# Kernel optimization log

Hardware: AMD Instinct MI355X
Metric: run time of the kernel (lower is better)

The kernel has to match this reference:

```python
import jax, jax.numpy as jnp
import numpy as np

D = 1  # dilation


def _unfold3x3(x, d):
    # x: [B, C, H, W] -> [B, H*W, 9, C]; matches torch.nn.Unfold(kernel_size=3,
    # dilation=d, padding=d, stride=1) followed by the module's reshapes.
    B, C, H, W = x.shape
    xp = jnp.pad(x, ((0, 0), (0, 0), (d, d), (d, d)))
    pats = [xp[:, :, i * d:i * d + H, j * d:j * d + W] for i in range(3) for j in range(3)]
    p = jnp.stack(pats, axis=0)  # [9, B, C, H, W], kernel positions row-major (center = 4)
    return p.transpose(1, 3, 4, 0, 2).reshape(B, H * W, 9, C)


def _masked_bn(h, m, gamma, beta, eps=1e-5):
    # BatchNorm1d in training mode applied only to rows selected by bool mask m
    # (the torch code gathers rows, BNs them, scatters back into zeros).
    # Stats are the biased mean/var over the selected rows, per channel.
    axes = tuple(range(h.ndim - 1))
    mf = m[..., None].astype(h.dtype)
    n = jnp.maximum(mf.sum(), 1.0)
    mean = (h * mf).sum(axes) / n
    var = (((h - mean) ** 2 * mf)).sum(axes) / n
    return (h - mean) * jax.lax.rsqrt(var + eps) * gamma + beta


def setup_inputs() -> dict:
    key = jax.random.key(0)
    ks = jax.random.split(key, 8)
    B, H, W = 2, 64, 1024
    Cin, Cout, Cm = 64, 64, 4
    s = 0.1
    x = jax.random.normal(ks[0], (B, Cm + Cin, H, W), jnp.float32)
    mask = (jax.random.uniform(ks[1], (B, 1, H, W)) > 0.3).astype(jnp.float32)
    return {
        "x": x,
        "mask": mask,
        "w1": jax.random.normal(ks[2], (8, Cm), jnp.float32) * s,
        "bn1_g": jnp.ones(8, jnp.float32),
        "bn1_b": jnp.zeros(8, jnp.float32),
        "w2": jax.random.normal(ks[3], (1, 8), jnp.float32) * s,
        "b2": jnp.zeros(1, jnp.float32),
        "g1": jax.random.normal(ks[4], (8, Cm), jnp.float32) * s,
        "gbn1_g": jnp.ones(8, jnp.float32),
        "gbn1_b": jnp.zeros(8, jnp.float32),
        "g2": jax.random.normal(ks[5], (8, 8), jnp.float32) * s,
        "gbn2_g": jnp.ones(8, jnp.float32),
        "gbn2_b": jnp.zeros(8, jnp.float32),
        "w_agg": jax.random.normal(ks[6], (Cout, 72 + Cin), jnp.float32) * s,
        "abn_g": jnp.ones(Cout, jnp.float32),
        "abn_b": jnp.zeros(Cout, jnp.float32),
    }


def reference(x, mask, w1, bn1_g, bn1_b, w2, b2, g1, gbn1_g, gbn1_b, g2, gbn2_g, gbn2_b, w_agg, abn_g, abn_b):
    B, C, H, W = x.shape
    xu = _unfold3x3(x, D)                      # [B, HW, 9, C]
    mu = _unfold3x3(mask, D)[..., 0]           # [B, HW, 9]
    msel = mu > 0                              # valid-neighbor mask
    mp0 = msel[:, :, 4]                        # valid-center mask [B, HW]
    pn = xu[..., :4] - xu[:, :, 4:5, :4]       # relative meta coords [B, HW, 9, 4]
    feats = xu[..., 4:]                        # neighbor features [B, HW, 9, Cin]

    # weight branch (dense compute + mask == torch's gather/scatter)
    h = _masked_bn(pn @ w1.T, msel, bn1_g, bn1_b)
    h = jax.nn.relu(h) @ w2.T + b2             # [B, HW, 9, 1]
    wts = jnp.where(msel, h[..., 0], 0.0)      # zeros at invalid neighbors pre-softmax
    wts = jax.nn.softmax(wts, axis=-1)[..., None]

    fagg = (wts * feats).sum(axis=2)           # [B, HW, Cin]

    # geo branch
    g = jax.nn.relu(_masked_bn(pn @ g1.T, msel, gbn1_g, gbn1_b))
    g = jax.nn.relu(_masked_bn(g @ g2.T, msel, gbn2_g, gbn2_b))
    g = jnp.where(msel[..., None], g, 0.0)
    g = (wts * g).reshape(B, H * W, 72)

    # aggregation over valid centers
    out = jnp.concatenate([fagg, g], axis=-1) @ w_agg.T
    out = jax.nn.relu(_masked_bn(out, mp0, abn_g, abn_b))
    out = jnp.where(mp0[..., None], out, 0.0)  # [B, HW, Cout]
    return out.transpose(0, 2, 1).reshape(B, -1, H, W)  # fold with k=1 == reshape
```

## Files before the change

kernel.cpp:

```cpp
#include <hip/hip_runtime.h>

#define HW_ 65536
#define W_ 1024
#define H_ 64
#define B_ 2
#define C_ 68
#define NPIX 131072
#define EPS 1e-5f

typedef __attribute__((ext_vector_type(8))) short short8;
typedef __attribute__((ext_vector_type(4))) float floatx4;

__device__ __forceinline__ unsigned short f2bf(float f) {
  unsigned u = __float_as_uint(f);
  u += 0x7fffu + ((u >> 16) & 1u);
  return (unsigned short)(u >> 16);
}
__device__ __forceinline__ unsigned pack2(float a, float b) {
  return (unsigned)f2bf(a) | ((unsigned)f2bf(b) << 16);
}
__device__ __forceinline__ float wred(float v) {
  v += __shfl_xor(v, 1);  v += __shfl_xor(v, 2);  v += __shfl_xor(v, 4);
  v += __shfl_xor(v, 8);  v += __shfl_xor(v, 16); v += __shfl_xor(v, 32);
  return v;
}
__device__ __forceinline__ int swz_tile(int bid) {
  return (bid & 7) * 64 + (bid >> 3);
}

__global__ __launch_bounds__(256) void k_stats1(
    const float* __restrict__ x, const float* __restrict__ mask,
    const float* __restrict__ w1, const float* __restrict__ g1,
    float* __restrict__ ws) {
  float acc[34];
#pragma unroll
  for (int i = 0; i < 34; i++) acc[i] = 0.f;

  int p = swz_tile(blockIdx.x) * 256 + threadIdx.x;
  {
    int b = p >> 16, s = p & (HW_ - 1);
    int h = s >> 10, w = s & (W_ - 1);
    const float* xb = x + (size_t)b * C_ * HW_;
    const float* mb = mask + (size_t)b * HW_;
    float xc0 = xb[s], xc1 = xb[HW_ + s], xc2 = xb[2 * HW_ + s], xc3 = xb[3 * HW_ + s];
    acc[33] += (mb[s] > 0.f) ? 1.f : 0.f;
#pragma unroll
    for (int k = 0; k < 9; k++) {
      int di = k / 3 - 1, dj = k % 3 - 1;
      int hh = h + di, ww = w + dj;
      bool inb = ((unsigned)hh < (unsigned)H_) && ((unsigned)ww < (unsigned)W_);
      int ns = hh * W_ + ww;
      float mval = inb ? mb[ns] : 0.f;
      if (mval > 0.f) {
        float pn0 = xb[ns] - xc0;
        float pn1 = xb[HW_ + ns] - xc1;
        float pn2 = xb[2 * HW_ + ns] - xc2;
        float pn3 = xb[3 * HW_ + ns] - xc3;
        acc[32] += 1.f;
#pragma unroll
        for (int o = 0; o < 8; o++) {
          float ta = pn0 * w1[o * 4] + pn1 * w1[o * 4 + 1] + pn2 * w1[o * 4 + 2] + pn3 * w1[o * 4 + 3];
          acc[o] += ta; acc[8 + o] += ta * ta;
          float tg = pn0 * g1[o * 4] + pn1 * g1[o * 4 + 1] + pn2 * g1[o * 4 + 2] + pn3 * g1[o * 4 + 3];
          acc[16 + o] += tg; acc[24 + o] += tg * tg;
        }
      }
    }
  }
  __shared__ float red[4][34];
  int lane = threadIdx.x & 63, wave = threadIdx.x >> 6;
#pragma unroll
  for (int i = 0; i < 34; i++) {
    float r = wred(acc[i]);
    if (lane == 0) red[wave][i] = r;
  }
  __syncthreads();
  if (threadIdx.x < 34)
    atomicAdd(&ws[threadIdx.x],
              red[0][threadIdx.x] + red[1][threadIdx.x] + red[2][threadIdx.x] + red[3][threadIdx.x]);
}

__global__ __launch_bounds__(256) void k_stats2(
    const float* __restrict__ x, const float* __restrict__ mask,
    const float* __restrict__ g1, const float* __restrict__ gbn1_g,
    const float* __restrict__ gbn1_b, const float* __restrict__ g2,
    float* __restrict__ ws) {
  __shared__ float sc[8], sh[8];
  if (threadIdx.x < 8) {
    int o = threadIdx.x;
    float n = fmaxf(ws[32], 1.f);
    float mean = ws[16 + o] / n;
    float var = ws[24 + o] / n - mean * mean;
    float s = gbn1_g[o] * rsqrtf(var + EPS);
    sc[o] = s; sh[o] = gbn1_b[o] - mean * s;
  }
  __syncthreads();

  float acc[16];
#pragma unroll
  for (int i = 0; i < 16; i++) acc[i] = 0.f;

  int p = swz_tile(blockIdx.x) * 256 + threadIdx.x;
  {
    int b = p >> 16, s = p & (HW_ - 1);
    int h = s >> 10, w = s & (W_ - 1);
    const float* xb = x + (size_t)b * C_ * HW_;
    const float* mb = mask + (size_t)b * HW_;
    float xc0 = xb[s], xc1 = xb[HW_ + s], xc2 = xb[2 * HW_ + s], xc3 = xb[3 * HW_ + s];
#pragma unroll
    for (int k = 0; k < 9; k++) {
      int di = k / 3 - 1, dj = k % 3 - 1;
      int hh = h + di, ww = w + dj;
      bool inb = ((unsigned)hh < (unsigned)H_) && ((unsigned)ww < (unsigned)W_);
      int ns = hh * W_ + ww;
      float mval = inb ? mb[ns] : 0.f;
      if (mval > 0.f) {
        float pn0 = xb[ns] - xc0;
        float pn1 = xb[HW_ + ns] - xc1;
        float pn2 = xb[2 * HW_ + ns] - xc2;
        float pn3 = xb[3 * HW_ + ns] - xc3;
        float gb[8];
#pragma unroll
        for (int o = 0; o < 8; o++) {
          float tg = pn0 * g1[o * 4] + pn1 * g1[o * 4 + 1] + pn2 * g1[o * 4 + 2] + pn3 * g1[o * 4 + 3];
          gb[o] = fmaxf(sc[o] * tg + sh[o], 0.f);
        }
#pragma unroll
        for (int j = 0; j < 8; j++) {
          float t2 = 0.f;
#pragma unroll
          for (int o = 0; o < 8; o++) t2 += gb[o] * g2[j * 8 + o];
          acc[j] += t2; acc[8 + j] += t2 * t2;
        }
      }
    }
  }
  __shared__ float red[4][16];
  int lane = threadIdx.x & 63, wave = threadIdx.x >> 6;
#pragma unroll
  for (int i = 0; i < 16; i++) {
    float r = wred(acc[i]);
    if (lane == 0) red[wave][i] = r;
  }
  __syncthreads();
  if (threadIdx.x < 16)
    atomicAdd(&ws[40 + threadIdx.x],
              red[0][threadIdx.x] + red[1][threadIdx.x] + red[2][threadIdx.x] + red[3][threadIdx.x]);
}

__global__ __launch_bounds__(256) void k_fused(
    const float* __restrict__ x, const float* __restrict__ mask,
    const float* __restrict__ w1, const float* __restrict__ bn1_g,
    const float* __restrict__ bn1_b, const float* __restrict__ w2,
    const float* __restrict__ b2, const float* __restrict__ g1,
    const float* __restrict__ gbn1_g, const float* __restrict__ gbn1_b,
    const float* __restrict__ g2, const float* __restrict__ gbn2_g,
    const float* __restrict__ gbn2_b, const float* __restrict__ w_agg,
    const float* __restrict__ ws, float* __restrict__ out_pre,
    float* __restrict__ wsum) {
  __shared__ uint4 vecA[17][256];
  __shared__ float sA[8], hA[8], sG1[8], hG1[8], sG2[8], hG2[8];

  if (threadIdx.x < 24) {
    int o = threadIdx.x & 7;
    float n = fmaxf(ws[32], 1.f);
    float sum, sum2, gma, bta;
    if (threadIdx.x < 8)       { sum = ws[o];      sum2 = ws[8 + o];  gma = bn1_g[o];  bta = bn1_b[o]; }
    else if (threadIdx.x < 16) { sum = ws[16 + o]; sum2 = ws[24 + o]; gma = gbn1_g[o]; bta = gbn1_b[o]; }
    else                       { sum = ws[40 + o]; sum2 = ws[48 + o]; gma = gbn2_g[o]; bta = gbn2_b[o]; }
    float mean = sum / n, var = sum2 / n - mean * mean;
    float s = gma * rsqrtf(var + EPS);
    float sft = bta - mean * s;
    if (threadIdx.x < 8)       { sA[o] = s;  hA[o] = sft; }
    else if (threadIdx.x < 16) { sG1[o] = s; hG1[o] = sft; }
    else                       { sG2[o] = s; hG2[o] = sft; }
  }
  __syncthreads();

  int tile = swz_tile(blockIdx.x);
  int p0 = tile * 256;
  int p = p0 + threadIdx.x;
  int b = p >> 16, s = p & (HW_ - 1);
  int h = s >> 10, w = s & (W_ - 1);
  const float* xb = x + (size_t)b * C_ * HW_;
  const float* mb = mask + (size_t)b * HW_;
  float xc0 = xb[s], xc1 = xb[HW_ + s], xc2 = xb[2 * HW_ + s], xc3 = xb[3 * HW_ + s];
  float b2v = b2[0];

  float ev[9]; int nsv[9]; bool inbv[9], mselv[9];
  float mx = -1e30f;
#pragma unroll
  for (int k = 0; k < 9; k++) {
    int di = k / 3 - 1, dj = k % 3 - 1;
    int hh = h + di, ww = w + dj;
    bool inb = ((unsigned)hh < (unsigned)H_) && ((unsigned)ww < (unsigned)W_);
    int ns = hh * W_ + ww;
    inbv[k] = inb; nsv[k] = ns;
    float mval = inb ? mb[ns] : 0.f;
    bool msel = mval > 0.f;
    mselv[k] = msel;
    float wp = 0.f;
    if (msel) {
      float pn0 = xb[ns] - xc0;
      float pn1 = xb[HW_ + ns] - xc1;
      float pn2 = xb[2 * HW_ + ns] - xc2;
      float pn3 = xb[3 * HW_ + ns] - xc3;
      float accw = 0.f;
#pragma unroll
      for (int o = 0; o < 8; o++) {
        float ta = pn0 * w1[o * 4] + pn1 * w1[o * 4 + 1] + pn2 * w1[o * 4 + 2] + pn3 * w1[o * 4 + 3];
        accw += fmaxf(sA[o] * ta + hA[o], 0.f) * w2[o];
      }
      wp = accw + b2v;
    }
    ev[k] = wp;
    mx = fmaxf(mx, wp);
  }
  float den = 0.f;
#pragma unroll
  for (int k = 0; k < 9; k++) { ev[k] = __expf(ev[k] - mx); den += ev[k]; }
  float inv = 1.f / den;

  float fagg[64];
#pragma unroll
  for (int c = 0; c < 64; c++) fagg[c] = 0.f;

#pragma unroll
  for (int k = 0; k < 9; k++) {
    float wt = ev[k] * inv;
    int ns = nsv[k];
    uint4 pk; pk.x = pk.y = pk.z = pk.w = 0u;
    if (mselv[k]) {
      float pn0 = xb[ns] - xc0;
      float pn1 = xb[HW_ + ns] - xc1;
      float pn2 = xb[2 * HW_ + ns] - xc2;
      float pn3 = xb[3 * HW_ + ns] - xc3;
      float gb[8];
#pragma unroll
      for (int o = 0; o < 8; o++) {
        float tg = pn0 * g1[o * 4] + pn1 * g1[o * 4 + 1] + pn2 * g1[o * 4 + 2] + pn3 * g1[o * 4 + 3];
        gb[o] = fmaxf(sG1[o] * tg + hG1[o], 0.f);
      }
      float gv[8];
#pragma unroll
      for (int j = 0; j < 8; j++) {
        float t2 = 0.f;
#pragma unroll
        for (int o = 0; o < 8; o++) t2 += gb[o] * g2[j * 8 + o];
        float gg = fmaxf(sG2[j] * t2 + hG2[j], 0.f);
        gv[j] = wt * gg;
      }
      pk.x = pack2(gv[0], gv[1]); pk.y = pack2(gv[2], gv[3]);
      pk.z = pack2(gv[4], gv[5]); pk.w = pack2(gv[6], gv[7]);
    }
    vecA[8 + k][threadIdx.x] = pk;
    if (inbv[k]) {
      const float* xf = xb + 4 * HW_ + ns;
#pragma unroll
      for (int c = 0; c < 64; c++) fagg[c] += wt * xf[c * HW_];
    }
  }
#pragma unroll
  for (int c = 0; c < 64; c += 8) {
    uint4 pk;
    pk.x = pack2(fagg[c], fagg[c + 1]);     pk.y = pack2(fagg[c + 2], fagg[c + 3]);
    pk.z = pack2(fagg[c + 4], fagg[c + 5]); pk.w = pack2(fagg[c + 6], fagg[c + 7]);
    vecA[c >> 3][threadIdx.x] = pk;
  }
  __syncthreads();

  int lane = threadIdx.x & 63, wave = threadIdx.x >> 6;
  int q = lane >> 4, r = lane & 15;

  short8 Bf[4][5];
#pragma unroll
  for (int nt = 0; nt < 4; nt++) {
    int n = nt * 16 + r;
#pragma unroll
    for (int ks = 0; ks < 5; ks++) {
      int k0 = ks * 32 + q * 8;
      uint4 pk; pk.x = pk.y = pk.z = pk.w = 0u;
      if (k0 < 136) {
        float4 f0 = *reinterpret_cast<const float4*>(w_agg + n * 136 + k0);
        float4 f1 = *reinterpret_cast<const float4*>(w_agg + n * 136 + k0 + 4);
        pk.x = pack2(f0.x, f0.y); pk.y = pack2(f0.z, f0.w);
        pk.z = pack2(f1.x, f1.y); pk.w = pack2(f1.z, f1.w);
      }
      Bf[nt][ks] = *reinterpret_cast<short8*>(&pk);
    }
  }

  floatx4 acc[4][4];
#pragma unroll
  for (int m = 0; m < 4; m++)
#pragma unroll
    for (int nt = 0; nt < 4; nt++) acc[m][nt] = (floatx4){0.f, 0.f, 0.f, 0.f};

#pragma unroll
  for (int m = 0; m < 4; m++) {
    int mt = wave * 4 + m;
    int pix = mt * 16 + r;
    short8 Af[5];
#pragma unroll
    for (int ks = 0; ks < 5; ks++) {
      int chunk = ks * 4 + q;
      if (chunk < 17)
        Af[ks] = *reinterpret_cast<const short8*>(&vecA[chunk][pix]);
      else
        Af[ks] = (short8){0, 0, 0, 0, 0, 0, 0, 0};
    }
#pragma unroll
    for (int nt = 0; nt < 4; nt++)
#pragma unroll
      for (int ks = 0; ks < 5; ks++)
        acc[m][nt] = __builtin_amdgcn_mfma_f32_16x16x32_bf16(Af[ks], Bf[nt][ks], acc[m][nt], 0, 0, 0);
  }

  float aS[4] = {0.f, 0.f, 0.f, 0.f}, aQ[4] = {0.f, 0.f, 0.f, 0.f};
  int s0 = p0 & (HW_ - 1);
#pragma unroll
  for (int m = 0; m < 4; m++) {
    int mt = wave * 4 + m;
    int srow = s0 + mt * 16 + q * 4;
    float4 mv = *reinterpret_cast<const float4*>(mb + srow);
    float m0 = (mv.x > 0.f) ? 1.f : 0.f, m1 = (mv.y > 0.f) ? 1.f : 0.f;
    float m2 = (mv.z > 0.f) ? 1.f : 0.f, m3 = (mv.w > 0.f) ? 1.f : 0.f;
#pragma unroll
    for (int nt = 0; nt < 4; nt++) {
      int ch = nt * 16 + r;
      float4 ov;
      ov.x = acc[m][nt][0]; ov.y = acc[m][nt][1];
      ov.z = acc[m][nt][2]; ov.w = acc[m][nt][3];
      aS[nt] += ov.x * m0 + ov.y * m1 + ov.z * m2 + ov.w * m3;
      aQ[nt] += ov.x * ov.x * m0 + ov.y * ov.y * m1 + ov.z * ov.z * m2 + ov.w * ov.w * m3;
      *reinterpret_cast<float4*>(out_pre + ((size_t)(b * 64 + ch)) * HW_ + srow) = ov;
    }
  }

  __syncthreads();
  float* rS = (float*)&vecA[0][0];
  float* rQ = rS + 256;
#pragma unroll
  for (int nt = 0; nt < 4; nt++) {
    float v1 = aS[nt], v2 = aQ[nt];
    v1 += __shfl_xor(v1, 16); v1 += __shfl_xor(v1, 32);
    v2 += __shfl_xor(v2, 16); v2 += __shfl_xor(v2, 32);
    if (lane < 16) { rS[wave * 64 + nt * 16 + lane] = v1; rQ[wave * 64 + nt * 16 + lane] = v2; }
  }
  __syncthreads();
  if (threadIdx.x < 64) {
    atomicAdd(&wsum[64 + threadIdx.x],
              rS[threadIdx.x] + rS[64 + threadIdx.x] + rS[128 + threadIdx.x] + rS[192 + threadIdx.x]);
    atomicAdd(&wsum[128 + threadIdx.x],
              rQ[threadIdx.x] + rQ[64 + threadIdx.x] + rQ[128 + threadIdx.x] + rQ[192 + threadIdx.x]);
  }
}

__global__ __launch_bounds__(256) void k_final(
    const float* __restrict__ out_pre, const float* __restrict__ mask,
    const float* __restrict__ abn_g, const float* __restrict__ abn_b,
    const float* __restrict__ ws, float* __restrict__ out) {
  __shared__ float sc[64], sh[64];
  if (threadIdx.x < 64) {
    int c = threadIdx.x;
    float n0 = fmaxf(ws[33], 1.f);
    float mean = ws[64 + c] / n0;
    float var = ws[128 + c] / n0 - mean * mean;
    float s = abn_g[c] * rsqrtf(var + EPS);
    sc[c] = s; sh[c] = abn_b[c] - mean * s;
  }
  __syncthreads();
  int i4 = (blockIdx.x * 256 + threadIdx.x) * 4;
  if (i4 >= B_ * 64 * HW_) return;
  int c = (i4 >> 16) & 63;
  int b = i4 >> 22;
  int s = i4 & (HW_ - 1);
  float4 v = *reinterpret_cast<const float4*>(out_pre + i4);
  float4 m = *reinterpret_cast<const float4*>(mask + (size_t)b * HW_ + s);
  float4 o;
  o.x = (m.x > 0.f) ? fmaxf(v.x * sc[c] + sh[c], 0.f) : 0.f;
  o.y = (m.y > 0.f) ? fmaxf(v.y * sc[c] + sh[c], 0.f) : 0.f;
  o.z = (m.z > 0.f) ? fmaxf(v.z * sc[c] + sh[c], 0.f) : 0.f;
  o.w = (m.w > 0.f) ? fmaxf(v.w * sc[c] + sh[c], 0.f) : 0.f;
  *reinterpret_cast<float4*>(out + i4) = o;
}

extern "C" void kernel_launch(void* const* d_in, const int* in_sizes, int n_in,
                              void* d_out, int out_size, void* d_ws, size_t ws_size,
                              hipStream_t stream) {
  const float* x      = (const float*)d_in[0];
  const float* mask   = (const float*)d_in[1];
  const float* w1     = (const float*)d_in[2];
  const float* bn1_g  = (const float*)d_in[3];
  const float* bn1_b  = (const float*)d_in[4];
  const float* w2     = (const float*)d_in[5];
  const float* b2     = (const float*)d_in[6];
  const float* g1     = (const float*)d_in[7];
  const float* gbn1_g = (const float*)d_in[8];
  const float* gbn1_b = (const float*)d_in[9];
  const float* g2     = (const float*)d_in[10];
  const float* gbn2_g = (const float*)d_in[11];
  const float* gbn2_b = (const float*)d_in[12];
  const float* w_agg  = (const float*)d_in[13];
  const float* abn_g  = (const float*)d_in[14];
  const float* abn_b  = (const float*)d_in[15];
  float* out = (float*)d_out;

  size_t need = 1024 + (size_t)NPIX * 64 * 4;
  if (ws_size < need) return;

  float* wsf = (float*)d_ws;
  float* out_pre = (float*)((char*)d_ws + 1024);

  hipMemsetAsync(d_ws, 0, 1024, stream);
  k_stats1<<<512, 256, 0, stream>>>(x, mask, w1, g1, wsf);
  k_stats2<<<512, 256, 0, stream>>>(x, mask, g1, gbn1_g, gbn1_b, g2, wsf);
  k_fused<<<512, 256, 0, stream>>>(x, mask, w1, bn1_g, bn1_b, w2, b2, g1,
                                   gbn1_g, gbn1_b, g2, gbn2_g, gbn2_b, w_agg,
                                   wsf, out_pre, wsf);
  k_final<<<8192, 256, 0, stream>>>(out_pre, mask, abn_g, abn_b, wsf, out);
}
```

Measured before the change: 222.9 us.

## Store intermediate in bf16, split fused tile across half-blocks, drop atomics for stats

Several changes at once. The pre-BN aggregation output is now stored as bf16 instead of fp32, halving that intermediate's write and read traffic. Stats kernels write per-block partials instead of atomics, and each block handles both batches for the same pixel. The masking branches become branchless multiply-by-mask. The fused kernel now uses 128-pixel tiles with two half-blocks splitting neighbor and channel work and the MFMA N dimension. The bf16 intermediate adds rounding error before batch norm, and the branchless form does extra arithmetic on invalid neighbors.

```diff
diff --git a/kernel.cpp b/kernel.cpp
--- a/kernel.cpp
+++ b/kernel.cpp
@@ -8,6 +8,7 @@
 #define NPIX 131072
 #define EPS 1e-5f
 
+
 typedef __attribute__((ext_vector_type(8))) short short8;
 typedef __attribute__((ext_vector_type(4))) float floatx4;
 
@@ -19,13 +20,13 @@
 __device__ __forceinline__ unsigned pack2(float a, float b) {
   return (unsigned)f2bf(a) | ((unsigned)f2bf(b) << 16);
 }
+__device__ __forceinline__ float bf2f(unsigned short u) {
+  return __uint_as_float(((unsigned)u) << 16);
+}
 __device__ __forceinline__ float wred(float v) {
   v += __shfl_xor(v, 1);  v += __shfl_xor(v, 2);  v += __shfl_xor(v, 4);
   v += __shfl_xor(v, 8);  v += __shfl_xor(v, 16); v += __shfl_xor(v, 32);
   return v;
-}
-__device__ __forceinline__ int swz_tile(int bid) {
-  return (bid & 7) * 64 + (bid >> 3);
 }
 
 __global__ __launch_bounds__(256) void k_stats1(
@@ -36,9 +37,11 @@
 #pragma unroll
   for (int i = 0; i < 34; i++) acc[i] = 0.f;
 
-  int p = swz_tile(blockIdx.x) * 256 + threadIdx.x;
-  {
-    int b = p >> 16, s = p & (HW_ - 1);
+  int t = blockIdx.x * 256 + threadIdx.x;
+#pragma unroll
+  for (int pp = 0; pp < 2; pp++) {
+    int s = t;
+    int b = pp;
     int h = s >> 10, w = s & (W_ - 1);
     const float* xb = x + (size_t)b * C_ * HW_;
     const float* mb = mask + (size_t)b * HW_;
@@ -49,21 +52,20 @@
       int di = k / 3 - 1, dj = k % 3 - 1;
       int hh = h + di, ww = w + dj;
       bool inb = ((unsigned)hh < (unsigned)H_) && ((unsigned)ww < (unsigned)W_);
-      int ns = hh * W_ + ww;
-      float mval = inb ? mb[ns] : 0.f;
-      if (mval > 0.f) {
-        float pn0 = xb[ns] - xc0;
-        float pn1 = xb[HW_ + ns] - xc1;
-        float pn2 = xb[2 * HW_ + ns] - xc2;
-        float pn3 = xb[3 * HW_ + ns] - xc3;
-        acc[32] += 1.f;
-#pragma unroll
-        for (int o = 0; o < 8; o++) {
-          float ta = pn0 * w1[o * 4] + pn1 * w1[o * 4 + 1] + pn2 * w1[o * 4 + 2] + pn3 * w1[o * 4 + 3];
-          acc[o] += ta; acc[8 + o] += ta * ta;
-          float tg = pn0 * g1[o * 4] + pn1 * g1[o * 4 + 1] + pn2 * g1[o * 4 + 2] + pn3 * g1[o * 4 + 3];
-          acc[16 + o] += tg; acc[24 + o] += tg * tg;
-        }
+      int ns = inb ? hh * W_ + ww : s;
+      float mv = mb[ns];
+      float mk = (inb && mv > 0.f) ? 1.f : 0.f;
+      float pn0 = xb[ns] - xc0;
+      float pn1 = xb[HW_ + ns] - xc1;
+      float pn2 = xb[2 * HW_ + ns] - xc2;
+      float pn3 = xb[3 * HW_ + ns] - xc3;
+      acc[32] += mk;
+#pragma unroll
+      for (int o = 0; o < 8; o++) {
+        float ta = pn0 * w1[o * 4] + pn1 * w1[o * 4 + 1] + pn2 * w1[o * 4 + 2] + pn3 * w1[o * 4 + 3];
+        acc[o] += mk * ta; acc[8 + o] += mk * ta * ta;
+        float tg = pn0 * g1[o * 4] + pn1 * g1[o * 4 + 1] + pn2 * g1[o * 4 + 2] + pn3 * g1[o * 4 + 3];
+        acc[16 + o] += mk * tg; acc[24 + o] += mk * tg * tg;
       }
     }
   }
@@ -76,8 +78,8 @@
   }
   __syncthreads();
   if (threadIdx.x < 34)
-    atomicAdd(&ws[threadIdx.x],
-              red[0][threadIdx.x] + red[1][threadIdx.x] + red[2][threadIdx.x] + red[3][threadIdx.x]);
+    ws[threadIdx.x * 256 + blockIdx.x] =
+        red[0][threadIdx.x] + red[1][threadIdx.x] + red[2][threadIdx.x] + red[3][threadIdx.x];
 }
 
 __global__ __launch_bounds__(256) void k_stats2(
@@ -85,12 +87,21 @@
     const float* __restrict__ g1, const float* __restrict__ gbn1_g,
     const float* __restrict__ gbn1_b, const float* __restrict__ g2,
     float* __restrict__ ws) {
+  int lane = threadIdx.x & 63, wave = threadIdx.x >> 6;
+  __shared__ float stat[33];
+  for (int i = 16 + wave; i < 33; i += 4) {
+    const float* src = ws + i * 256;
+    float v = src[lane] + src[64 + lane] + src[128 + lane] + src[192 + lane];
+    v = wred(v);
+    if (lane == 0) stat[i] = v;
+  }
+  __syncthreads();
   __shared__ float sc[8], sh[8];
   if (threadIdx.x < 8) {
     int o = threadIdx.x;
-    float n = fmaxf(ws[32], 1.f);
-    float mean = ws[16 + o] / n;
-    float var = ws[24 + o] / n - mean * mean;
+    float n = fmaxf(stat[32], 1.f);
+    float mean = stat[16 + o] / n;
+    float var = stat[24 + o] / n - mean * mean;
     float s = gbn1_g[o] * rsqrtf(var + EPS);
     sc[o] = s; sh[o] = gbn1_b[o] - mean * s;
   }
@@ -100,9 +111,11 @@
 #pragma unroll
   for (int i = 0; i < 16; i++) acc[i] = 0.f;
 
-  int p = swz_tile(blockIdx.x) * 256 + threadIdx.x;
-  {
-    int b = p >> 16, s = p & (HW_ - 1);
+  int t = blockIdx.x * 256 + threadIdx.x;
+#pragma unroll
+  for (int pp = 0; pp < 2; pp++) {
+    int s = t;
+    int b = pp;
     int h = s >> 10, w = s & (W_ - 1);
     const float* xb = x + (size_t)b * C_ * HW_;
     const float* mb = mask + (size_t)b * HW_;
@@ -112,31 +125,29 @@
       int di = k / 3 - 1, dj = k % 3 - 1;
       int hh = h + di, ww = w + dj;
       bool inb = ((unsigned)hh < (unsigned)H_) && ((unsigned)ww < (unsigned)W_);
-      int ns = hh * W_ + ww;
-      float mval = inb ? mb[ns] : 0.f;
-      if (mval > 0.f) {
-        float pn0 = xb[ns] - xc0;
-        float pn1 = xb[HW_ + ns] - xc1;
-        float pn2 = xb[2 * HW_ + ns] - xc2;
-        float pn3 = xb[3 * HW_ + ns] - xc3;
-        float gb[8];
-#pragma unroll
-        for (int o = 0; o < 8; o++) {
-          float tg = pn0 * g1[o * 4] + pn1 * g1[o * 4 + 1] + pn2 * g1[o * 4 + 2] + pn3 * g1[o * 4 + 3];
-          gb[o] = fmaxf(sc[o] * tg + sh[o], 0.f);
-        }
-#pragma unroll
-        for (int j = 0; j < 8; j++) {
-          float t2 = 0.f;
-#pragma unroll
-          for (int o = 0; o < 8; o++) t2 += gb[o] * g2[j * 8 + o];
-          acc[j] += t2; acc[8 + j] += t2 * t2;
-        }
+      int ns = inb ? hh * W_ + ww : s;
+      float mv = mb[ns];
+      float mk = (inb && mv > 0.f) ? 1.f : 0.f;
+      float pn0 = xb[ns] - xc0;
+      float pn1 = xb[HW_ + ns] - xc1;
+      float pn2 = xb[2 * HW_ + ns] - xc2;
+      float pn3 = xb[3 * HW_ + ns] - xc3;
+      float gb[8];
+#pragma unroll
+      for (int o = 0; o < 8; o++) {
+        float tg = pn0 * g1[o * 4] + pn1 * g1[o * 4 + 1] + pn2 * g1[o * 4 + 2] + pn3 * g1[o * 4 + 3];
+        gb[o] = fmaxf(sc[o] * tg + sh[o], 0.f);
+      }
+#pragma unroll
+      for (int j = 0; j < 8; j++) {
+        float t2 = 0.f;
+#pragma unroll
+        for (int o = 0; o < 8; o++) t2 += gb[o] * g2[j * 8 + o];
+        acc[j] += mk * t2; acc[8 + j] += mk * t2 * t2;
       }
     }
   }
   __shared__ float red[4][16];
-  int lane = threadIdx.x & 63, wave = threadIdx.x >> 6;
 #pragma unroll
   for (int i = 0; i < 16; i++) {
     float r = wred(acc[i]);
@@ -144,8 +155,8 @@
   }
   __syncthreads();
   if (threadIdx.x < 16)
-    atomicAdd(&ws[40 + threadIdx.x],
-              red[0][threadIdx.x] + red[1][threadIdx.x] + red[2][threadIdx.x] + red[3][threadIdx.x]);
+    ws[8704 + threadIdx.x * 256 + blockIdx.x] =
+        red[0][threadIdx.x] + red[1][threadIdx.x] + red[2][threadIdx.x] + red[3][threadIdx.x];
 }
 
 __global__ __launch_bounds__(256) void k_fused(
@@ -153,21 +164,29 @@
     const float* __restrict__ w1, const float* __restrict__ bn1_g,
     const float* __restrict__ bn1_b, const float* __restrict__ w2,
     const float* __restrict__ b2, const float* __restrict__ g1,
-    const float* __restrict__ gbn1_g, const float* __restrict__ gbn1_b,
-    const float* __restrict__ g2, const float* __restrict__ gbn2_g,
+    const float* __restrict__ g2, const float* __restrict__ gbn1_g,
+    const float* __restrict__ gbn1_b, const float* __restrict__ gbn2_g,
     const float* __restrict__ gbn2_b, const float* __restrict__ w_agg,
-    const float* __restrict__ ws, float* __restrict__ out_pre,
-    float* __restrict__ wsum) {
-  __shared__ uint4 vecA[17][256];
+    float* __restrict__ ws, unsigned short* __restrict__ out_pre) {
+  __shared__ uint4 vecT[17][128];
+  __shared__ float stat[50];
   __shared__ float sA[8], hA[8], sG1[8], hG1[8], sG2[8], hG2[8];
 
+  int lane = threadIdx.x & 63, wave = threadIdx.x >> 6;
+  for (int i = wave; i < 50; i += 4) {
+    const float* src = (i < 34) ? (ws + i * 256) : (ws + 8704 + (i - 34) * 256);
+    float v = src[lane] + src[64 + lane] + src[128 + lane] + src[192 + lane];
+    v = wred(v);
+    if (lane == 0) stat[i] = v;
+  }
+  __syncthreads();
   if (threadIdx.x < 24) {
     int o = threadIdx.x & 7;
-    float n = fmaxf(ws[32], 1.f);
+    float n = fmaxf(stat[32], 1.f);
     float sum, sum2, gma, bta;
-    if (threadIdx.x < 8)       { sum = ws[o];      sum2 = ws[8 + o];  gma = bn1_g[o];  bta = bn1_b[o]; }
-    else if (threadIdx.x < 16) { sum = ws[16 + o]; sum2 = ws[24 + o]; gma = gbn1_g[o]; bta = gbn1_b[o]; }
-    else                       { sum = ws[40 + o]; sum2 = ws[48 + o]; gma = gbn2_g[o]; bta = gbn2_b[o]; }
+    if (threadIdx.x < 8)       { sum = stat[o];      sum2 = stat[8 + o];  gma = bn1_g[o];  bta = bn1_b[o]; }
+    else if (threadIdx.x < 16) { sum = stat[16 + o]; sum2 = stat[24 + o]; gma = gbn1_g[o]; bta = gbn1_b[o]; }
+    else                       { sum = stat[34 + o]; sum2 = stat[42 + o]; gma = gbn2_g[o]; bta = gbn2_b[o]; }
     float mean = sum / n, var = sum2 / n - mean * mean;
     float s = gma * rsqrtf(var + EPS);
     float sft = bta - mean * s;
@@ -177,42 +196,42 @@
   }
   __syncthreads();
 
-  int tile = swz_tile(blockIdx.x);
-  int p0 = tile * 256;
-  int p = p0 + threadIdx.x;
-  int b = p >> 16, s = p & (HW_ - 1);
+  int tile = (blockIdx.x & 7) * 128 + (blockIdx.x >> 3);
+  int b = tile >> 9;
+  int s0 = (tile & 511) * 128;
+  int px = threadIdx.x & 127;
+  int half = threadIdx.x >> 7;
+  int s = s0 + px;
   int h = s >> 10, w = s & (W_ - 1);
   const float* xb = x + (size_t)b * C_ * HW_;
   const float* mb = mask + (size_t)b * HW_;
   float xc0 = xb[s], xc1 = xb[HW_ + s], xc2 = xb[2 * HW_ + s], xc3 = xb[3 * HW_ + s];
   float b2v = b2[0];
 
-  float ev[9]; int nsv[9]; bool inbv[9], mselv[9];
+  float ev[9], mkv[9], ibv[9]; int nsv[9];
   float mx = -1e30f;
 #pragma unroll
   for (int k = 0; k < 9; k++) {
     int di = k / 3 - 1, dj = k % 3 - 1;
     int hh = h + di, ww = w + dj;
     bool inb = ((unsigned)hh < (unsigned)H_) && ((unsigned)ww < (unsigned)W_);
-    int ns = hh * W_ + ww;
-    inbv[k] = inb; nsv[k] = ns;
-    float mval = inb ? mb[ns] : 0.f;
-    bool msel = mval > 0.f;
-    mselv[k] = msel;
-    float wp = 0.f;
-    if (msel) {
-      float pn0 = xb[ns] - xc0;
-      float pn1 = xb[HW_ + ns] - xc1;
-      float pn2 = xb[2 * HW_ + ns] - xc2;
-      float pn3 = xb[3 * HW_ + ns] - xc3;
-      float accw = 0.f;
-#pragma unroll
-      for (int o = 0; o < 8; o++) {
-        float ta = pn0 * w1[o * 4] + pn1 * w1[o * 4 + 1] + pn2 * w1[o * 4 + 2] + pn3 * w1[o * 4 + 3];
-        accw += fmaxf(sA[o] * ta + hA[o], 0.f) * w2[o];
-      }
-      wp = accw + b2v;
-    }
+    int ns = inb ? hh * W_ + ww : s;
+    nsv[k] = ns;
+    ibv[k] = inb ? 1.f : 0.f;
+    float mv = mb[ns];
+    float mk = (inb && mv > 0.f) ? 1.f : 0.f;
+    mkv[k] = mk;
+    float pn0 = xb[ns] - xc0;
+    float pn1 = xb[HW_ + ns] - xc1;
+    float pn2 = xb[2 * HW_ + ns] - xc2;
+    float pn3 = xb[3 * HW_ + ns] - xc3;
+    float accw = 0.f;
+#pragma unroll
+    for (int o = 0; o < 8; o++) {
+      float ta = pn0 * w1[o * 4] + pn1 * w1[o * 4 + 1] + pn2 * w1[o * 4 + 2] + pn3 * w1[o * 4 + 3];
+      accw += fmaxf(sA[o] * ta + hA[o], 0.f) * w2[o];
+    }
+    float wp = mk * (accw + b2v);
     ev[k] = wp;
     mx = fmaxf(mx, wp);
   }
@@ -220,17 +239,18 @@
 #pragma unroll
   for (int k = 0; k < 9; k++) { ev[k] = __expf(ev[k] - mx); den += ev[k]; }
   float inv = 1.f / den;
-
-  float fagg[64];
-#pragma unroll
-  for (int c = 0; c < 64; c++) fagg[c] = 0.f;
-
+  float wgv[9], wfv[9];
 #pragma unroll
   for (int k = 0; k < 9; k++) {
     float wt = ev[k] * inv;
-    int ns = nsv[k];
-    uint4 pk; pk.x = pk.y = pk.z = pk.w = 0u;
-    if (mselv[k]) {
+    wgv[k] = wt * mkv[k];
+    wfv[k] = wt * ibv[k];
+  }
+
+#pragma unroll
+  for (int k = 0; k < 9; k++) {
+    if ((k < 4) == (half == 0)) {
+      int ns = nsv[k];
       float pn0 = xb[ns] - xc0;
       float pn1 = xb[HW_ + ns] - xc1;
       float pn2 = xb[2 * HW_ + ns] - xc2;
@@ -241,41 +261,49 @@
         float tg = pn0 * g1[o * 4] + pn1 * g1[o * 4 + 1] + pn2 * g1[o * 4 + 2] + pn3 * g1[o * 4 + 3];
         gb[o] = fmaxf(sG1[o] * tg + hG1[o], 0.f);
       }
+      float wg = wgv[k];
       float gv[8];
 #pragma unroll
       for (int j = 0; j < 8; j++) {
         float t2 = 0.f;
 #pragma unroll
         for (int o = 0; o < 8; o++) t2 += gb[o] * g2[j * 8 + o];
-        float gg = fmaxf(sG2[j] * t2 + hG2[j], 0.f);
-        gv[j] = wt * gg;
-      }
+        gv[j] = wg * fmaxf(sG2[j] * t2 + hG2[j], 0.f);
+      }
+      uint4 pk;
       pk.x = pack2(gv[0], gv[1]); pk.y = pack2(gv[2], gv[3]);
       pk.z = pack2(gv[4], gv[5]); pk.w = pack2(gv[6], gv[7]);
-    }
-    vecA[8 + k][threadIdx.x] = pk;
-    if (inbv[k]) {
-      const float* xf = xb + 4 * HW_ + ns;
-#pragma unroll
-      for (int c = 0; c < 64; c++) fagg[c] += wt * xf[c * HW_];
-    }
-  }
-#pragma unroll
-  for (int c = 0; c < 64; c += 8) {
+      vecT[8 + k][px] = pk;
+    }
+  }
+
+  float fa[32];
+#pragma unroll
+  for (int c = 0; c < 32; c++) fa[c] = 0.f;
+  const float* xf0 = xb + (size_t)(4 + half * 32) * HW_;
+#pragma unroll
+  for (int k = 0; k < 9; k++) {
+    float wf = wfv[k];
+    const float* xf = xf0 + nsv[k];
+#pragma unroll
+    for (int c = 0; c < 32; c++) fa[c] += wf * xf[c * HW_];
+  }
+#pragma unroll
+  for (int c = 0; c < 32; c += 8) {
     uint4 pk;
-    pk.x = pack2(fagg[c], fagg[c + 1]);     pk.y = pack2(fagg[c + 2], fagg[c + 3]);
-    pk.z = pack2(fagg[c + 4], fagg[c + 5]); pk.w = pack2(fagg[c + 6], fagg[c + 7]);
-    vecA[c >> 3][threadIdx.x] = pk;
-  }
-  __syncthreads();
-
-  int lane = threadIdx.x & 63, wave = threadIdx.x >> 6;
+    pk.x = pack2(fa[c], fa[c + 1]);     pk.y = pack2(fa[c + 2], fa[c + 3]);
+    pk.z = pack2(fa[c + 4], fa[c + 5]); pk.w = pack2(fa[c + 6], fa[c + 7]);
+    vecT[half * 4 + (c >> 3)][px] = pk;
+  }
+  __syncthreads();
+
   int q = lane >> 4, r = lane & 15;
-
-  short8 Bf[4][5];
-#pragma unroll
-  for (int nt = 0; nt < 4; nt++) {
-    int n = nt * 16 + r;
+  int nh = wave & 1, mh = wave >> 1;
+
+  short8 Bf[2][5];
+#pragma unroll
+  for (int nt = 0; nt < 2; nt++) {
+    int n = (nh * 2 + nt) * 16 + r;
 #pragma unroll
     for (int ks = 0; ks < 5; ks++) {
       int k0 = ks * 32 + q * 8;
@@ -290,99 +318,110 @@
     }
   }
 
-  floatx4 acc[4][4];
+  floatx4 acc[4][2];
 #pragma unroll
   for (int m = 0; m < 4; m++)
 #pragma unroll
-    for (int nt = 0; nt < 4; nt++) acc[m][nt] = (floatx4){0.f, 0.f, 0.f, 0.f};
+    for (int nt = 0; nt < 2; nt++) acc[m][nt] = (floatx4){0.f, 0.f, 0.f, 0.f};
 
 #pragma unroll
   for (int m = 0; m < 4; m++) {
-    int mt = wave * 4 + m;
-    int pix = mt * 16 + r;
+    int pix = (mh * 4 + m) * 16 + r;
     short8 Af[5];
 #pragma unroll
     for (int ks = 0; ks < 5; ks++) {
-      int chunk = ks * 4 + q;
-      if (chunk < 17)
-        Af[ks] = *reinterpret_cast<const short8*>(&vecA[chunk][pix]);
+      int ch = ks * 4 + q;
+      if (ch < 17)
+        Af[ks] = *reinterpret_cast<const short8*>(&vecT[ch][pix]);
       else
         Af[ks] = (short8){0, 0, 0, 0, 0, 0, 0, 0};
     }
 #pragma unroll
-    for (int nt = 0; nt < 4; nt++)
+    for (int nt = 0; nt < 2; nt++)
 #pragma unroll
       for (int ks = 0; ks < 5; ks++)
         acc[m][nt] = __builtin_amdgcn_mfma_f32_16x16x32_bf16(Af[ks], Bf[nt][ks], acc[m][nt], 0, 0, 0);
   }
 
-  float aS[4] = {0.f, 0.f, 0.f, 0.f}, aQ[4] = {0.f, 0.f, 0.f, 0.f};
-  int s0 = p0 & (HW_ - 1);
+  float aS[2] = {0.f, 0.f}, aQ[2] = {0.f, 0.f};
 #pragma unroll
   for (int m = 0; m < 4; m++) {
-    int mt = wave * 4 + m;
-    int srow = s0 + mt * 16 + q * 4;
+    int srow = s0 + (mh * 4 + m) * 16 + q * 4;
     float4 mv = *reinterpret_cast<const float4*>(mb + srow);
     float m0 = (mv.x > 0.f) ? 1.f : 0.f, m1 = (mv.y > 0.f) ? 1.f : 0.f;
     float m2 = (mv.z > 0.f) ? 1.f : 0.f, m3 = (mv.w > 0.f) ? 1.f : 0.f;
 #pragma unroll
-    for (int nt = 0; nt < 4; nt++) {
-      int ch = nt * 16 + r;
-      float4 ov;
-      ov.x = acc[m][nt][0]; ov.y = acc[m][nt][1];
-      ov.z = acc[m][nt][2]; ov.w = acc[m][nt][3];
-      aS[nt] += ov.x * m0 + ov.y * m1 + ov.z * m2 + ov.w * m3;
-      aQ[nt] += ov.x * ov.x * m0 + ov.y * ov.y * m1 + ov.z * ov.z * m2 + ov.w * ov.w * m3;
-      *reinterpret_cast<float4*>(out_pre + ((size_t)(b * 64 + ch)) * HW_ + srow) = ov;
-    }
-  }
-
-  __syncthreads();
-  float* rS = (float*)&vecA[0][0];
-  float* rQ = rS + 256;
-#pragma unroll
-  for (int nt = 0; nt < 4; nt++) {
+    for (int nt = 0; nt < 2; nt++) {
+      int ch = (nh * 2 + nt) * 16 + r;
+      float o0 = acc[m][nt][0], o1 = acc[m][nt][1], o2 = acc[m][nt][2], o3 = acc[m][nt][3];
+      aS[nt] += o0 * m0 + o1 * m1 + o2 * m2 + o3 * m3;
+      aQ[nt] += o0 * o0 * m0 + o1 * o1 * m1 + o2 * o2 * m2 + o3 * o3 * m3;
+      uint2 pk;
+      pk.x = pack2(o0, o1); pk.y = pack2(o2, o3);
+      *reinterpret_cast<uint2*>(out_pre + (size_t)(b * 64 + ch) * HW_ + srow) = pk;
+    }
+  }
+
+  __shared__ float rS[4][32], rQ[4][32];
+#pragma unroll
+  for (int nt = 0; nt < 2; nt++) {
     float v1 = aS[nt], v2 = aQ[nt];
     v1 += __shfl_xor(v1, 16); v1 += __shfl_xor(v1, 32);
     v2 += __shfl_xor(v2, 16); v2 += __shfl_xor(v2, 32);
-    if (lane < 16) { rS[wave * 64 + nt * 16 + lane] = v1; rQ[wave * 64 + nt * 16 + lane] = v2; }
+    if (lane < 16) { rS[wave][nt * 16 + lane] = v1; rQ[wave][nt * 16 + lane] = v2; }
   }
   __syncthreads();
   if (threadIdx.x < 64) {
-    atomicAdd(&wsum[64 + threadIdx.x],
-              rS[threadIdx.x] + rS[64 + threadIdx.x] + rS[128 + threadIdx.x] + rS[192 + threadIdx.x]);
-    atomicAdd(&wsum[128 + threadIdx.x],
-              rQ[threadIdx.x] + rQ[64 + threadIdx.x] + rQ[128 + threadIdx.x] + rQ[192 + threadIdx.x]);
+    int nh2 = threadIdx.x >> 5, loc = threadIdx.x & 31;
+    float* AT = ws + 12800;
+    atomicAdd(&AT[threadIdx.x], rS[nh2][loc] + rS[2 + nh2][loc]);
+    atomicAdd(&AT[64 + threadIdx.x], rQ[nh2][loc] + rQ[2 + nh2][loc]);
   }
 }
 
 __global__ __launch_bounds__(256) void k_final(
-    const float* __restrict__ out_pre, const float* __restrict__ mask,
+    const unsigned short* __restrict__ out_pre, const float* __restrict__ mask,
     const float* __restrict__ abn_g, const float* __restrict__ abn_b,
     const float* __restrict__ ws, float* __restrict__ out) {
+  int lane = threadIdx.x & 63, wave = threadIdx.x >> 6;
+  __shared__ float l4[4];
   __shared__ float sc[64], sh[64];
+  {
+    float v = ws[33 * 256 + threadIdx.x];
+    v = wred(v);
+    if (lane == 0) l4[wave] = v;
+  }
+  __syncthreads();
+  float n0 = fmaxf(l4[0] + l4[1] + l4[2] + l4[3], 1.f);
   if (threadIdx.x < 64) {
     int c = threadIdx.x;
-    float n0 = fmaxf(ws[33], 1.f);
-    float mean = ws[64 + c] / n0;
-    float var = ws[128 + c] / n0 - mean * mean;
+    const float* AT = ws + 12800;
+    float mean = AT[c] / n0;
+    float var = AT[64 + c] / n0 - mean * mean;
     float s = abn_g[c] * rsqrtf(var + EPS);
     sc[c] = s; sh[c] = abn_b[c] - mean * s;
   }
   __syncthreads();
-  int i4 = (blockIdx.x * 256 + threadIdx.x) * 4;
-  if (i4 >= B_ * 64 * HW_) return;
-  int c = (i4 >> 16) & 63;
-  int b = i4 >> 22;
-  int s = i4 & (HW_ - 1);
-  float4 v = *reinterpret_cast<const float4*>(out_pre + i4);
-  float4 m = *reinterpret_cast<const float4*>(mask + (size_t)b * HW_ + s);
-  float4 o;
-  o.x = (m.x > 0.f) ? fmaxf(v.x * sc[c] + sh[c], 0.f) : 0.f;
-  o.y = (m.y > 0.f) ? fmaxf(v.y * sc[c] + sh[c], 0.f) : 0.f;
-  o.z = (m.z > 0.f) ? fmaxf(v.z * sc[c] + sh[c], 0.f) : 0.f;
-  o.w = (m.w > 0.f) ? fmaxf(v.w * sc[c] + sh[c], 0.f) : 0.f;
-  *reinterpret_cast<float4*>(out + i4) = o;
+
+  int i8 = (blockIdx.x * 256 + threadIdx.x) * 8;
+  int c = (i8 >> 16) & 63;
+  int b = i8 >> 22;
+  int s = i8 & (HW_ - 1);
+  uint4 v = *reinterpret_cast<const uint4*>(out_pre + i8);
+  float4 ma = *reinterpret_cast<const float4*>(mask + (size_t)b * HW_ + s);
+  float4 mb4 = *reinterpret_cast<const float4*>(mask + (size_t)b * HW_ + s + 4);
+  float scc = sc[c], shc = sh[c];
+  float4 o0, o1;
+  o0.x = (ma.x > 0.f) ? fmaxf(bf2f((unsigned short)(v.x & 0xffff)) * scc + shc, 0.f) : 0.f;
+  o0.y = (ma.y > 0.f) ? fmaxf(bf2f((unsigned short)(v.x >> 16)) * scc + shc, 0.f) : 0.f;
+  o0.z = (ma.z > 0.f) ? fmaxf(bf2f((unsigned short)(v.y & 0xffff)) * scc + shc, 0.f) : 0.f;
+  o0.w = (ma.w > 0.f) ? fmaxf(bf2f((unsigned short)(v.y >> 16)) * scc + shc, 0.f) : 0.f;
+  o1.x = (mb4.x > 0.f) ? fmaxf(bf2f((unsigned short)(v.z & 0xffff)) * scc + shc, 0.f) : 0.f;
+  o1.y = (mb4.y > 0.f) ? fmaxf(bf2f((unsigned short)(v.z >> 16)) * scc + shc, 0.f) : 0.f;
+  o1.z = (mb4.z > 0.f) ? fmaxf(bf2f((unsigned short)(v.w & 0xffff)) * scc + shc, 0.f) : 0.f;
+  o1.w = (mb4.w > 0.f) ? fmaxf(bf2f((unsigned short)(v.w >> 16)) * scc + shc, 0.f) : 0.f;
+  *reinterpret_cast<float4*>(out + i8) = o0;
+  *reinterpret_cast<float4*>(out + i8 + 4) = o1;
 }
 
 extern "C" void kernel_launch(void* const* d_in, const int* in_sizes, int n_in,
@@ -406,17 +445,17 @@
   const float* abn_b  = (const float*)d_in[15];
   float* out = (float*)d_out;
 
-  size_t need = 1024 + (size_t)NPIX * 64 * 4;
+  size_t need = 53248 + (size_t)NPIX * 64 * 2;
   if (ws_size < need) return;
 
   float* wsf = (float*)d_ws;
-  float* out_pre = (float*)((char*)d_ws + 1024);
-
-  hipMemsetAsync(d_ws, 0, 1024, stream);
-  k_stats1<<<512, 256, 0, stream>>>(x, mask, w1, g1, wsf);
-  k_stats2<<<512, 256, 0, stream>>>(x, mask, g1, gbn1_g, gbn1_b, g2, wsf);
-  k_fused<<<512, 256, 0, stream>>>(x, mask, w1, bn1_g, bn1_b, w2, b2, g1,
-                                   gbn1_g, gbn1_b, g2, gbn2_g, gbn2_b, w_agg,
-                                   wsf, out_pre, wsf);
-  k_final<<<8192, 256, 0, stream>>>(out_pre, mask, abn_g, abn_b, wsf, out);
-}
+  unsigned short* out_pre = (unsigned short*)((char*)d_ws + 53248);
+
+  hipMemsetAsync((char*)d_ws + 51200, 0, 1024, stream);
+  k_stats1<<<256, 256, 0, stream>>>(x, mask, w1, g1, wsf);
+  k_stats2<<<256, 256, 0, stream>>>(x, mask, g1, gbn1_g, gbn1_b, g2, wsf);
+  k_fused<<<1024, 256, 0, stream>>>(x, mask, w1, bn1_g, bn1_b, w2, b2, g1, g2,
+                                    gbn1_g, gbn1_b, gbn2_g, gbn2_b, w_agg,
+                                    wsf, out_pre);
+  k_final<<<4096, 256, 0, stream>>>(out_pre, mask, abn_g, abn_b, wsf, out);
+}
```

Result: slower. 262.0 us (+17.5%).
